# Performance work log

Hardware: AMD Instinct MI355X
Metric: run time of the kernel (lower is better)

The kernel has to match this reference:

```python
import jax, jax.numpy as jnp
import numpy as np

DIM = 768
HEADS = 12
SCALE = DIM ** -0.5  # NOTE: module scales by full dim, not head dim


def setup_inputs() -> dict:
    key = jax.random.key(0)
    ks = jax.random.split(key, 5)
    B, N, C = 8, 1024, DIM
    x = jax.random.normal(ks[0], (B, N, C), dtype=jnp.float32)
    W_qkv = jax.random.normal(ks[1], (C, 3 * C), dtype=jnp.float32) * (C ** -0.5)
    b_qkv = jnp.zeros((3 * C,), dtype=jnp.float32)
    W_out = jax.random.normal(ks[2], (C, C), dtype=jnp.float32) * (C ** -0.5)
    b_out = jnp.zeros((C,), dtype=jnp.float32)
    return {"x": x, "W_qkv": W_qkv, "b_qkv": b_qkv, "W_out": W_out, "b_out": b_out}


def reference(x, W_qkv, b_qkv, W_out, b_out) -> jnp.ndarray:
    B, N, C = x.shape
    H, D = HEADS, C // HEADS
    qkv = x @ W_qkv + b_qkv                       # [B, N, 3C]
    q, k, v = jnp.split(qkv, 3, axis=-1)
    # [B, N, C] -> [B, H, N, D]
    q = q.reshape(B, N, H, D).transpose(0, 2, 1, 3)
    k = k.reshape(B, N, H, D).transpose(0, 2, 1, 3)
    v = v.reshape(B, N, H, D).transpose(0, 2, 1, 3)
    attn = jnp.einsum("bhnd,bhmd->bhnm", q, k) * SCALE
    attn = jax.nn.softmax(attn, axis=-1)
    out = jnp.einsum("bhnm,bhmd->bhnd", attn, v)   # [B, H, N, D]
    out = out.transpose(0, 2, 1, 3).reshape(B, N, C)
    return out @ W_out + b_out
```

## Files before the change

### kernel.cpp

```cpp
#include <hip/hip_runtime.h>
#include <hip/hip_bf16.h>

typedef __attribute__((ext_vector_type(4))) float f32x4;
typedef __attribute__((ext_vector_type(4))) unsigned u32x4;
typedef __attribute__((ext_vector_type(8))) short bf16x8;

#define QSCALE  (0.03608439182435161f * 1.44269504088896f)

__device__ __forceinline__ unsigned short f2bf(float f) {
    union { float f; unsigned u; } v; v.f = f;
    return (unsigned short)((v.u + 0x7FFFu + ((v.u >> 16) & 1u)) >> 16);
}

__device__ __forceinline__ float fast_exp2(float x) {
#if __has_builtin(__builtin_amdgcn_exp2f)
    return __builtin_amdgcn_exp2f(x);
#else
    return exp2f(x);
#endif
}

__device__ __forceinline__ void gload_lds16(const void* g, void* l) {
    __builtin_amdgcn_global_load_lds(
        (const __attribute__((address_space(1))) unsigned int*)g,
        (__attribute__((address_space(3))) unsigned int*)l, 16, 0, 0);
}

__global__ __launch_bounds__(256) void prep_kernel(
    const float* __restrict__ X, unsigned short* __restrict__ Xb,
    const float* __restrict__ Wqkv, unsigned short* __restrict__ WqkvT,
    const float* __restrict__ Wout, unsigned short* __restrict__ WoutT)
{
    __shared__ unsigned short T[64][68];
    const int bid = blockIdx.x, t = threadIdx.x;

    if (bid < 3072) {
        const int i = bid * 256 + t;
        f32x4 a = *(const f32x4*)(X + (size_t)i * 8);
        f32x4 b = *(const f32x4*)(X + (size_t)i * 8 + 4);
        bf16x8 w;
#pragma unroll
        for (int j = 0; j < 4; ++j) { w[j] = (short)f2bf(a[j]); w[4 + j] = (short)f2bf(b[j]); }
        *(bf16x8*)(Xb + (size_t)i * 8) = w;
        return;
    }

    const float* W; unsigned short* WT; int C, bx, by;
    if (bid < 3504) { W = Wqkv; WT = WqkvT; C = 2304; const int x = bid - 3072; bx = x % 36; by = x / 36; }
    else            { W = Wout; WT = WoutT; C = 768;  const int x = bid - 3504; bx = x % 12; by = x / 12; }
    const int R = 768;
    const int r0 = by * 64, c0 = bx * 64;
    {
        const int lr = t >> 4, lc = (t & 15) * 4;
#pragma unroll
        for (int p = 0; p < 4; ++p) {
            const float* s = W + (size_t)(r0 + lr + p * 16) * C + c0 + lc;
            f32x4 v = *(const f32x4*)s;
            unsigned short* d = &T[lr + p * 16][lc];
            d[0] = f2bf(v[0]); d[1] = f2bf(v[1]); d[2] = f2bf(v[2]); d[3] = f2bf(v[3]);
        }
    }
    __syncthreads();
    {
        const int oc = t >> 3, j0 = (t & 7) * 8;
#pragma unroll
        for (int p = 0; p < 2; ++p) {
            const int c = oc + p * 32;
            bf16x8 v;
#pragma unroll
            for (int j = 0; j < 8; ++j) v[j] = (short)T[j0 + j][c];
            *(bf16x8*)(WT + (size_t)(c0 + c) * R + r0 + j0) = v;
        }
    }
}

__global__ __launch_bounds__(256) void qkv_gemm_kernel(
    const unsigned short* __restrict__ Xb, const unsigned short* __restrict__ WT,
    const float* __restrict__ bias,
    unsigned short* __restrict__ Qw, unsigned short* __restrict__ Kw,
    unsigned short* __restrict__ VTw)
{
    __shared__ unsigned short SMEM[64 * 136 + 64];
    unsigned short* Alds = SMEM;
    unsigned short* Blds = SMEM + 128 * 32;

    const int t = threadIdx.x;
    const int lane = t & 63, wave = t >> 6;
    const int l15 = lane & 15, l4 = lane >> 4;
    const int m0 = blockIdx.x * 128, n0 = blockIdx.y * 64;
    const int wr = wave >> 1, wc = wave & 1;

    f32x4 acc[4][2];
#pragma unroll
    for (int m = 0; m < 4; ++m)
#pragma unroll
        for (int n = 0; n < 2; ++n) acc[m][n] = (f32x4){0.f, 0.f, 0.f, 0.f};

    for (int k0 = 0; k0 < 768; k0 += 32) {
#pragma unroll
        for (int c = 0; c < 2; ++c) {
            const int o = wave * 1024 + lane * 16 + c * 4096;
            const int row = o >> 6, cb = o & 63;
            gload_lds16((const char*)(Xb + (size_t)(m0 + row) * 768 + k0) + cb,
                        (char*)Alds + wave * 1024 + c * 4096);
        }
        {
            const int o = t * 16;
            const int row = o >> 6, cb = o & 63;
            gload_lds16((const char*)(WT + (size_t)(n0 + row) * 768 + k0) + cb,
                        (char*)Blds + o);
        }
        __syncthreads();
        bf16x8 af[4], bfr[2];
#pragma unroll
        for (int m = 0; m < 4; ++m)
            af[m] = *(const bf16x8*)((const char*)Alds + (wr * 64 + m * 16 + l15) * 64 + l4 * 16);
#pragma unroll
        for (int n = 0; n < 2; ++n)
            bfr[n] = *(const bf16x8*)((const char*)Blds + (wc * 32 + n * 16 + l15) * 64 + l4 * 16);
#pragma unroll
        for (int m = 0; m < 4; ++m)
#pragma unroll
            for (int n = 0; n < 2; ++n)
                acc[m][n] = __builtin_amdgcn_mfma_f32_16x16x32_bf16(af[m], bfr[n], acc[m][n], 0, 0, 0);
        __syncthreads();
    }

    if (n0 < 1536) {
        const int which = n0 / 768;
#pragma unroll
        for (int n = 0; n < 2; ++n) {
            const int col = n0 + wc * 32 + n * 16 + l15;
            const float bv = bias[col];
            const int cc = col - which * 768;
            const int h = cc >> 6, dd = cc & 63;
#pragma unroll
            for (int m = 0; m < 4; ++m) {
#pragma unroll
                for (int r = 0; r < 4; ++r) {
                    const int row = m0 + wr * 64 + m * 16 + l4 * 4 + r;
                    const int b = row >> 10, ntok = row & 1023;
                    const size_t bh = (size_t)b * 12 + h;
                    float val = acc[m][n][r] + bv;
                    if (which == 0) val *= QSCALE;
                    const unsigned short hv = f2bf(val);
                    if (which == 0) Qw[(bh * 1024 + ntok) * 64 + dd] = hv;
                    else            Kw[(bh * 1024 + ntok) * 64 + dd] = hv;
                }
            }
        }
    } else {
        const int b = m0 >> 10, ntok0 = m0 & 1023;
        const int h = (n0 - 1536) >> 6;
#pragma unroll
        for (int n = 0; n < 2; ++n) {
            const int cloc = wc * 32 + n * 16 + l15;
            const float bv = bias[n0 + cloc];
#pragma unroll
            for (int m = 0; m < 4; ++m)
#pragma unroll
                for (int r = 0; r < 4; ++r) {
                    const int ntl = wr * 64 + m * 16 + l4 * 4 + r;
                    SMEM[cloc * 136 + ntl] = f2bf(acc[m][n][r] + bv);
                }
        }
        __syncthreads();
        {
            const int sub = t & 15;
#pragma unroll
            for (int rep = 0; rep < 4; ++rep) {
                const int cll = rep * 16 + (t >> 4);
                const size_t rb = ((size_t)(b * 12 + h) * 64 + cll) * 1024 + ntok0 + sub * 8;
                *(bf16x8*)&VTw[rb] = *(const bf16x8*)&SMEM[cll * 136 + sub * 8];
            }
        }
    }
}

__global__ __launch_bounds__(256) void attn_kernel(
    const unsigned short* __restrict__ Qw, const unsigned short* __restrict__ Kw,
    const unsigned short* __restrict__ VTw, unsigned short* __restrict__ A2)
{
    __shared__ unsigned short Klds[2 * 64 * 64];
    __shared__ unsigned short Vlds[2 * 64 * 64];
    __shared__ float Flds[4 * 2 * 16];

    const int t = threadIdx.x, lane = t & 63, wave = t >> 6;
    const int l15 = lane & 15, l4 = lane >> 4;
    const int wg = (blockIdx.x & 7) * 96 + (blockIdx.x >> 3);
    const int qt = wg & 7, bh = wg >> 3;
    const int q0 = qt * 128;

    const size_t kvbase = (size_t)bh * 1024 * 64;
    const size_t vtbase = (size_t)bh * 64 * 1024;

    bf16x8 qf[2][2];
#pragma unroll
    for (int qs = 0; qs < 2; ++qs) {
        const unsigned short* qptr = Qw + kvbase + (size_t)(q0 + qs * 64 + wave * 16 + l15) * 64;
        qf[qs][0] = *(const bf16x8*)((const char*)qptr + l4 * 16);
        qf[qs][1] = *(const bf16x8*)((const char*)qptr + 64 + l4 * 16);
    }

    f32x4 oacc[2][4];
#pragma unroll
    for (int qs = 0; qs < 2; ++qs)
#pragma unroll
        for (int d = 0; d < 4; ++d) oacc[qs][d] = (f32x4){0.f, 0.f, 0.f, 0.f};
    float m_run[2] = {-1e30f, -1e30f}, l_run[2] = {0.f, 0.f};

    auto STAGE = [&](int kt, int bufi) {
        const int kv0 = kt * 64;
        char* kb = (char*)Klds + bufi * 8192;
        char* vb = (char*)Vlds + bufi * 8192;
#pragma unroll
        for (int c = 0; c < 2; ++c) {
            const int oo = wave * 1024 + lane * 16 + c * 4096;
            const int R = oo >> 7, w = oo & 127;
            const int sw = w ^ ((R & 7) << 4);
            const int kvs = (R & 0x23) | ((R & 0x0C) << 1) | ((R & 0x10) >> 2);
            gload_lds16((const char*)(Kw + kvbase + (size_t)(kv0 + kvs) * 64) + sw,
                        kb + wave * 1024 + c * 4096);
            gload_lds16((const char*)(VTw + vtbase + (size_t)R * 1024 + kv0) + sw,
                        vb + wave * 1024 + c * 4096);
        }
    };

    STAGE(0, 0);
    for (int kt = 0; kt < 16; ++kt) {
        const int cur = kt & 1;
        if (kt < 15) {
            STAGE(kt + 1, cur ^ 1);
            asm volatile("s_waitcnt vmcnt(4)" ::: "memory");
        } else {
            asm volatile("s_waitcnt vmcnt(0)" ::: "memory");
        }
        __builtin_amdgcn_s_barrier();
        __builtin_amdgcn_sched_barrier(0);
        const char* kb = (const char*)Klds + cur * 8192;
        const char* vb = (const char*)Vlds + cur * 8192;

#pragma unroll
        for (int qs = 0; qs < 2; ++qs) {
            f32x4 sacc[4];
#pragma unroll
            for (int i = 0; i < 4; ++i) sacc[i] = (f32x4){0.f, 0.f, 0.f, 0.f};
            __builtin_amdgcn_s_setprio(1);
#pragma unroll
            for (int ks = 0; ks < 2; ++ks) {
                const bf16x8 qq = qf[qs][ks];
#pragma unroll
                for (int kvf = 0; kvf < 4; ++kvf) {
                    const int row = kvf * 16 + l15;
                    int addr = row * 128 + ks * 64 + l4 * 16;
                    addr ^= (row & 7) << 4;
                    const bf16x8 kf = *(const bf16x8*)(kb + addr);
                    sacc[kvf] = __builtin_amdgcn_mfma_f32_16x16x32_bf16(kf, qq, sacc[kvf], 0, 0, 0);
                }
            }
            __builtin_amdgcn_s_setprio(0);

            float p[16];
            float tmax = -1e30f;
#pragma unroll
            for (int i = 0; i < 4; ++i)
#pragma unroll
                for (int r = 0; r < 4; ++r) {
                    p[i * 4 + r] = sacc[i][r];
                    tmax = fmaxf(tmax, sacc[i][r]);
                }
            tmax = fmaxf(tmax, __shfl_xor(tmax, 16));
            tmax = fmaxf(tmax, __shfl_xor(tmax, 32));

            if (!__all(tmax - m_run[qs] <= 8.f)) {
                const float mnew = fmaxf(m_run[qs], tmax);
                const float alpha = fast_exp2(m_run[qs] - mnew);
                m_run[qs] = mnew;
                if (lane < 16) Flds[wave * 32 + qs * 16 + lane] = alpha;
                const f32x4 av = *(const f32x4*)(&Flds[wave * 32 + qs * 16 + l4 * 4]);
#pragma unroll
                for (int d = 0; d < 4; ++d)
#pragma unroll
                    for (int r = 0; r < 4; ++r) oacc[qs][d][r] *= av[r];
                l_run[qs] *= alpha;
            }

            float tsum = 0.f;
#pragma unroll
            for (int i = 0; i < 16; ++i) { p[i] = fast_exp2(p[i] - m_run[qs]); tsum += p[i]; }
            tsum += __shfl_xor(tsum, 16);
            tsum += __shfl_xor(tsum, 32);
            l_run[qs] += tsum;

            bf16x8 paf[2];
#pragma unroll
            for (int ks = 0; ks < 2; ++ks) {
                union { u32x4 u; bf16x8 h; } cv;
#pragma unroll
                for (int j2 = 0; j2 < 4; ++j2)
                    asm("v_cvt_pk_bf16_f32 %0, %1, %2"
                        : "=v"(cv.u[j2]) : "v"(p[ks * 8 + 2 * j2]), "v"(p[ks * 8 + 2 * j2 + 1]));
                paf[ks] = cv.h;
            }

            __builtin_amdgcn_s_setprio(1);
#pragma unroll
            for (int ks = 0; ks < 2; ++ks) {
#pragma unroll
                for (int df = 0; df < 4; ++df) {
                    const int d = df * 16 + l15;
                    int addr = d * 128 + ks * 64 + l4 * 16;
                    addr ^= (d & 7) << 4;
                    const bf16x8 vf = *(const bf16x8*)(vb + addr);
                    oacc[qs][df] = __builtin_amdgcn_mfma_f32_16x16x32_bf16(paf[ks], vf, oacc[qs][df], 0, 0, 0);
                }
            }
            __builtin_amdgcn_s_setprio(0);
        }
        __builtin_amdgcn_s_barrier();
    }

    const int b = bh / 12, h = bh - b * 12;
#pragma unroll
    for (int qs = 0; qs < 2; ++qs) {
        if (lane < 16) Flds[wave * 32 + qs * 16 + lane] = 1.f / l_run[qs];
        const f32x4 inv = *(const f32x4*)(&Flds[wave * 32 + qs * 16 + l4 * 4]);
#pragma unroll
        for (int df = 0; df < 4; ++df) {
#pragma unroll
            for (int r = 0; r < 4; ++r) {
                const int row = b * 1024 + q0 + qs * 64 + wave * 16 + l4 * 4 + r;
                const int col = h * 64 + df * 16 + l15;
                A2[(size_t)row * 768 + col] = f2bf(oacc[qs][df][r] * inv[r]);
            }
        }
    }
}

__global__ __launch_bounds__(256) void out_gemm_kernel(
    const unsigned short* __restrict__ A2, const unsigned short* __restrict__ WT,
    const float* __restrict__ bias, float* __restrict__ Out)
{
    __shared__ unsigned short Alds[128 * 32];
    __shared__ unsigned short Blds[64 * 32];

    const int t = threadIdx.x;
    const int lane = t & 63, wave = t >> 6;
    const int l15 = lane & 15, l4 = lane >> 4;
    const int m0 = blockIdx.x * 128, n0 = blockIdx.y * 64;
    const int wr = wave >> 1, wc = wave & 1;

    f32x4 acc[4][2];
#pragma unroll
    for (int m = 0; m < 4; ++m)
#pragma unroll
        for (int n = 0; n < 2; ++n) acc[m][n] = (f32x4){0.f, 0.f, 0.f, 0.f};

    for (int k0 = 0; k0 < 768; k0 += 32) {
#pragma unroll
        for (int c = 0; c < 2; ++c) {
            const int o = wave * 1024 + lane * 16 + c * 4096;
            const int row = o >> 6, cb = o & 63;
            gload_lds16((const char*)(A2 + (size_t)(m0 + row) * 768 + k0) + cb,
                        (char*)Alds + wave * 1024 + c * 4096);
        }
        {
            const int o = t * 16;
            const int row = o >> 6, cb = o & 63;
            gload_lds16((const char*)(WT + (size_t)(n0 + row) * 768 + k0) + cb,
                        (char*)Blds + o);
        }
        __syncthreads();
        bf16x8 af[4], bfr[2];
#pragma unroll
        for (int m = 0; m < 4; ++m)
            af[m] = *(const bf16x8*)((const char*)Alds + (wr * 64 + m * 16 + l15) * 64 + l4 * 16);
#pragma unroll
        for (int n = 0; n < 2; ++n)
            bfr[n] = *(const bf16x8*)((const char*)Blds + (wc * 32 + n * 16 + l15) * 64 + l4 * 16);
#pragma unroll
        for (int m = 0; m < 4; ++m)
#pragma unroll
            for (int n = 0; n < 2; ++n)
                acc[m][n] = __builtin_amdgcn_mfma_f32_16x16x32_bf16(af[m], bfr[n], acc[m][n], 0, 0, 0);
        __syncthreads();
    }

#pragma unroll
    for (int n = 0; n < 2; ++n) {
        const int col = n0 + wc * 32 + n * 16 + l15;
        const float bv = bias[col];
#pragma unroll
        for (int m = 0; m < 4; ++m)
#pragma unroll
            for (int r = 0; r < 4; ++r) {
                const int row = m0 + wr * 64 + m * 16 + l4 * 4 + r;
                Out[(size_t)row * 768 + col] = acc[m][n][r] + bv;
            }
    }
}

extern "C" void kernel_launch(void* const* d_in, const int* in_sizes, int n_in,
                              void* d_out, int out_size, void* d_ws, size_t ws_size,
                              hipStream_t stream) {
    const float* X    = (const float*)d_in[0];
    const float* Wqkv = (const float*)d_in[1];
    const float* bqkv = (const float*)d_in[2];
    const float* Wout = (const float*)d_in[3];
    const float* bout = (const float*)d_in[4];
    float* Out = (float*)d_out;

    const size_t nq = (size_t)96 * 1024 * 64;
    unsigned short* XbA2  = (unsigned short*)d_ws;
    unsigned short* Qw    = XbA2 + nq;
    unsigned short* Kw    = Qw + nq;
    unsigned short* VTw   = Kw + nq;
    unsigned short* WqkvT = VTw + nq;
    unsigned short* WoutT = WqkvT + (size_t)2304 * 768;

    hipLaunchKernelGGL(prep_kernel, dim3(3648), dim3(256), 0, stream,
                       X, XbA2, Wqkv, WqkvT, Wout, WoutT);
    hipLaunchKernelGGL(qkv_gemm_kernel, dim3(64, 36), dim3(256), 0, stream,
                       XbA2, WqkvT, bqkv, Qw, Kw, VTw);
    hipLaunchKernelGGL(attn_kernel, dim3(768), dim3(256), 0, stream,
                       Qw, Kw, VTw, XbA2);
    hipLaunchKernelGGL(out_gemm_kernel, dim3(64, 12), dim3(256), 0, stream,
                       XbA2, WoutT, bout, Out);
}
```

Before: 125.5 us.

## Fuse X fp32-to-bf16 conversion into QKV GEMM A-tile loads

Removes the separate X conversion pass from the prep kernel. The QKV GEMM now loads fp32 X tiles directly into swizzled LDS and converts them to bf16 in registers with v_cvt_pk_bf16_f32 before the MFMAs. This drops one full write and read of a bf16 copy of X and shrinks the prep launch. In exchange, the GEMM reads twice the A bytes per tile (fp32), and each of the 36 column blocks re-reads and re-converts X. It also adds s_setprio around the MFMA block.

Measured after the change: 135.8 us. 1.08x slower.

```diff
diff --git a/kernel.cpp b/kernel.cpp
--- a/kernel.cpp
+++ b/kernel.cpp
@@ -27,27 +27,15 @@
 }
 
 __global__ __launch_bounds__(256) void prep_kernel(
-    const float* __restrict__ X, unsigned short* __restrict__ Xb,
     const float* __restrict__ Wqkv, unsigned short* __restrict__ WqkvT,
     const float* __restrict__ Wout, unsigned short* __restrict__ WoutT)
 {
     __shared__ unsigned short T[64][68];
     const int bid = blockIdx.x, t = threadIdx.x;
 
-    if (bid < 3072) {
-        const int i = bid * 256 + t;
-        f32x4 a = *(const f32x4*)(X + (size_t)i * 8);
-        f32x4 b = *(const f32x4*)(X + (size_t)i * 8 + 4);
-        bf16x8 w;
-#pragma unroll
-        for (int j = 0; j < 4; ++j) { w[j] = (short)f2bf(a[j]); w[4 + j] = (short)f2bf(b[j]); }
-        *(bf16x8*)(Xb + (size_t)i * 8) = w;
-        return;
-    }
-
     const float* W; unsigned short* WT; int C, bx, by;
-    if (bid < 3504) { W = Wqkv; WT = WqkvT; C = 2304; const int x = bid - 3072; bx = x % 36; by = x / 36; }
-    else            { W = Wout; WT = WoutT; C = 768;  const int x = bid - 3504; bx = x % 12; by = x / 12; }
+    if (bid < 432) { W = Wqkv; WT = WqkvT; C = 2304; bx = bid % 36; by = bid / 36; }
+    else           { W = Wout; WT = WoutT; C = 768;  const int x = bid - 432; bx = x % 12; by = x / 12; }
     const int R = 768;
     const int r0 = by * 64, c0 = bx * 64;
     {
@@ -75,14 +63,13 @@
 }
 
 __global__ __launch_bounds__(256) void qkv_gemm_kernel(
-    const unsigned short* __restrict__ Xb, const unsigned short* __restrict__ WT,
+    const float* __restrict__ X, const unsigned short* __restrict__ WT,
     const float* __restrict__ bias,
     unsigned short* __restrict__ Qw, unsigned short* __restrict__ Kw,
     unsigned short* __restrict__ VTw)
 {
-    __shared__ unsigned short SMEM[64 * 136 + 64];
-    unsigned short* Alds = SMEM;
-    unsigned short* Blds = SMEM + 128 * 32;
+    __shared__ __align__(16) char SMEM[20480];
+    unsigned short* Blds = (unsigned short*)(SMEM + 16384);
 
     const int t = threadIdx.x;
     const int lane = t & 63, wave = t >> 6;
@@ -96,13 +83,24 @@
 #pragma unroll
         for (int n = 0; n < 2; ++n) acc[m][n] = (f32x4){0.f, 0.f, 0.f, 0.f};
 
+    int aoff0[4], aoff1[4];
+#pragma unroll
+    for (int m = 0; m < 4; ++m) {
+        const int row = wr * 64 + m * 16 + l15;
+        const int sw = (row & 7) << 4;
+        aoff0[m] = (row * 128 + l4 * 32) ^ sw;
+        aoff1[m] = (row * 128 + l4 * 32 + 16) ^ sw;
+    }
+
     for (int k0 = 0; k0 < 768; k0 += 32) {
 #pragma unroll
-        for (int c = 0; c < 2; ++c) {
-            const int o = wave * 1024 + lane * 16 + c * 4096;
-            const int row = o >> 6, cb = o & 63;
-            gload_lds16((const char*)(Xb + (size_t)(m0 + row) * 768 + k0) + cb,
-                        (char*)Alds + wave * 1024 + c * 4096);
+        for (int c = 0; c < 4; ++c) {
+            const int base = wave * 4096 + c * 1024;
+            const int oo = base + lane * 16;
+            const int row = oo >> 7, w = oo & 127;
+            const int sw = w ^ ((row & 7) << 4);
+            gload_lds16((const char*)(X + (size_t)(m0 + row) * 768 + k0) + sw,
+                        SMEM + base);
         }
         {
             const int o = t * 16;
@@ -111,18 +109,29 @@
                         (char*)Blds + o);
         }
         __syncthreads();
+
         bf16x8 af[4], bfr[2];
 #pragma unroll
-        for (int m = 0; m < 4; ++m)
-            af[m] = *(const bf16x8*)((const char*)Alds + (wr * 64 + m * 16 + l15) * 64 + l4 * 16);
+        for (int m = 0; m < 4; ++m) {
+            const f32x4 a0 = *(const f32x4*)(SMEM + aoff0[m]);
+            const f32x4 a1 = *(const f32x4*)(SMEM + aoff1[m]);
+            union { u32x4 u; bf16x8 h; } cv;
+            asm("v_cvt_pk_bf16_f32 %0, %1, %2" : "=v"(cv.u[0]) : "v"(a0[0]), "v"(a0[1]));
+            asm("v_cvt_pk_bf16_f32 %0, %1, %2" : "=v"(cv.u[1]) : "v"(a0[2]), "v"(a0[3]));
+            asm("v_cvt_pk_bf16_f32 %0, %1, %2" : "=v"(cv.u[2]) : "v"(a1[0]), "v"(a1[1]));
+            asm("v_cvt_pk_bf16_f32 %0, %1, %2" : "=v"(cv.u[3]) : "v"(a1[2]), "v"(a1[3]));
+            af[m] = cv.h;
+        }
 #pragma unroll
         for (int n = 0; n < 2; ++n)
             bfr[n] = *(const bf16x8*)((const char*)Blds + (wc * 32 + n * 16 + l15) * 64 + l4 * 16);
+        __builtin_amdgcn_s_setprio(1);
 #pragma unroll
         for (int m = 0; m < 4; ++m)
 #pragma unroll
             for (int n = 0; n < 2; ++n)
                 acc[m][n] = __builtin_amdgcn_mfma_f32_16x16x32_bf16(af[m], bfr[n], acc[m][n], 0, 0, 0);
+        __builtin_amdgcn_s_setprio(0);
         __syncthreads();
     }
 
@@ -150,6 +159,7 @@
             }
         }
     } else {
+        unsigned short* EPI = (unsigned short*)SMEM;
         const int b = m0 >> 10, ntok0 = m0 & 1023;
         const int h = (n0 - 1536) >> 6;
 #pragma unroll
@@ -161,7 +171,7 @@
 #pragma unroll
                 for (int r = 0; r < 4; ++r) {
                     const int ntl = wr * 64 + m * 16 + l4 * 4 + r;
-                    SMEM[cloc * 136 + ntl] = f2bf(acc[m][n][r] + bv);
+                    EPI[cloc * 136 + ntl] = f2bf(acc[m][n][r] + bv);
                 }
         }
         __syncthreads();
@@ -171,7 +181,7 @@
             for (int rep = 0; rep < 4; ++rep) {
                 const int cll = rep * 16 + (t >> 4);
                 const size_t rb = ((size_t)(b * 12 + h) * 64 + cll) * 1024 + ntok0 + sub * 8;
-                *(bf16x8*)&VTw[rb] = *(const bf16x8*)&SMEM[cll * 136 + sub * 8];
+                *(bf16x8*)&VTw[rb] = *(const bf16x8*)&EPI[cll * 136 + sub * 8];
             }
         }
     }
@@ -411,19 +421,19 @@
     float* Out = (float*)d_out;
 
     const size_t nq = (size_t)96 * 1024 * 64;
-    unsigned short* XbA2  = (unsigned short*)d_ws;
-    unsigned short* Qw    = XbA2 + nq;
+    unsigned short* A2    = (unsigned short*)d_ws;
+    unsigned short* Qw    = A2 + nq;
     unsigned short* Kw    = Qw + nq;
     unsigned short* VTw   = Kw + nq;
     unsigned short* WqkvT = VTw + nq;
     unsigned short* WoutT = WqkvT + (size_t)2304 * 768;
 
-    hipLaunchKernelGGL(prep_kernel, dim3(3648), dim3(256), 0, stream,
-                       X, XbA2, Wqkv, WqkvT, Wout, WoutT);
+    hipLaunchKernelGGL(prep_kernel, dim3(576), dim3(256), 0, stream,
+                       Wqkv, WqkvT, Wout, WoutT);
     hipLaunchKernelGGL(qkv_gemm_kernel, dim3(64, 36), dim3(256), 0, stream,
-                       XbA2, WqkvT, bqkv, Qw, Kw, VTw);
+                       X, WqkvT, bqkv, Qw, Kw, VTw);
     hipLaunchKernelGGL(attn_kernel, dim3(768), dim3(256), 0, stream,
-                       Qw, Kw, VTw, XbA2);
+                       Qw, Kw, VTw, A2);
     hipLaunchKernelGGL(out_gemm_kernel, dim3(64, 12), dim3(256), 0, stream,
-                       XbA2, WoutT, bout, Out);
-}
+                       A2, WoutT, bout, Out);
+}
```
